# Optimization experiments

Measured on AMD Instinct MI355X. Metric: run time of the kernel, lower is better.

Reference implementation:

```python
import jax, jax.numpy as jnp
import numpy as np

D, H, FFN_D, B, LT, LS = 1024, 16, 4096, 4, 1024, 1024
EPS = 1e-5  # torch LayerNorm default
NEG = -10000000000.0


def setup_inputs() -> dict:
    key = jax.random.key(0)
    ks = iter(jax.random.split(key, 64))
    s = 0.02
    n = lambda shape: jax.random.normal(next(ks), shape, jnp.float32) * s
    inp = {
        'enc_output': n((LS, B, D)),
        'embedded': n((LT, B, D)),
        'src_mask': jnp.zeros((LS, B), jnp.bool_),
        'tgt_mask': jnp.zeros((LT, B), jnp.bool_),
    }
    for p in ('mmha', 'ed'):
        for w in ('q', 'k', 'v', 'o'):
            inp[f'{p}_w{w}'] = n((D, D))
            inp[f'{p}_b{w}'] = jnp.zeros((D,), jnp.float32)
    inp['ffn_w1'] = n((FFN_D, D)); inp['ffn_b1'] = jnp.zeros((FFN_D,), jnp.float32)
    inp['ffn_w2'] = n((D, FFN_D)); inp['ffn_b2'] = jnp.zeros((D,), jnp.float32)
    for i in range(3):
        inp[f'ln{i}_g'] = jnp.ones((D,), jnp.float32)
        inp[f'ln{i}_b'] = jnp.zeros((D,), jnp.float32)
    return inp


def _ln(x, g, b):
    m = x.mean(-1, keepdims=True)
    v = ((x - m) ** 2).mean(-1, keepdims=True)
    return (x - m) / jnp.sqrt(v + EPS) * g + b


def _mha(qx, kx, vx, wq, bq, wk, bk, wv, bv, wo, bo, mask):
    # qx: (Lq,B,D); kx,vx: (Lk,B,D); mask broadcastable to (B,H,Lq,Lk), True=masked
    Lq, Bn, Dm = qx.shape
    dk = Dm // H
    proj = lambda x, w, bb: (x @ w.T + bb).reshape(x.shape[0], Bn, H, dk).transpose(1, 2, 0, 3)
    q, k, v = proj(qx, wq, bq), proj(kx, wk, bk), proj(vx, wv, bv)  # (B,H,L,dk)
    scores = jnp.einsum('bhqd,bhkd->bhqk', q, k) / np.float32(np.sqrt(dk))
    scores = jnp.where(mask, NEG, scores)  # masked_fill semantics
    w = jax.nn.softmax(scores, axis=-1)  # dropout is identity in eval
    attn = jnp.einsum('bhqk,bhkd->bhqd', w, v).transpose(2, 0, 1, 3).reshape(Lq, Bn, Dm)
    return attn @ wo.T + bo


def reference(enc_output, embedded, src_mask, tgt_mask,
              mmha_wq, mmha_bq, mmha_wk, mmha_bk, mmha_wv, mmha_bv, mmha_wo, mmha_bo,
              ed_wq, ed_bq, ed_wk, ed_bk, ed_wv, ed_bv, ed_wo, ed_bo,
              ffn_w1, ffn_b1, ffn_w2, ffn_b2,
              ln0_g, ln0_b, ln1_g, ln1_b, ln2_g, ln2_b):
    Lt = embedded.shape[0]
    causal = jnp.triu(jnp.ones((Lt, Lt), jnp.bool_), 1)[None, None]      # (1,1,Lt,Lt)
    tmask = tgt_mask.T[:, None, None, :]                                  # (B,1,1,Lt)
    # Sublayer 0: masked self-attention (computed but UNUSED downstream,
    # faithfully mirroring the original forward which discards self_attn).
    self_attn = embedded + _mha(_ln(embedded, ln0_g, ln0_b), _ln(embedded, ln0_g, ln0_b), _ln(embedded, ln0_g, ln0_b),
                                mmha_wq, mmha_bq, mmha_wk, mmha_bk, mmha_wv, mmha_bv, mmha_wo, mmha_bo,
                                causal | tmask)
    del self_attn
    # Sublayer 1: enc-dec attention; residual input is `embedded` (as in source).
    smask = src_mask.T[:, None, None, :]                                  # (B,1,1,Ls)
    q_in = _ln(embedded, ln1_g, ln1_b)
    enc_dec = embedded + _mha(q_in, enc_output, enc_output,
                              ed_wq, ed_bq, ed_wk, ed_bk, ed_wv, ed_bv, ed_wo, ed_bo,
                              smask)
    # Sublayer 2: FFN
    z = _ln(enc_dec, ln2_g, ln2_b)
    ffn = jnp.maximum(z @ ffn_w1.T + ffn_b1, 0.0) @ ffn_w2.T + ffn_b2
    return enc_dec + ffn
```

## Files before the change

### kernel.cpp

```cpp
#include <hip/hip_runtime.h>
#include <cstdint>
#include <math.h>

constexpr int NH  = 16;
constexpr int DKH = 64;
constexpr int SEQ = 1024;
constexpr int NB  = 4;
constexpr int DM  = 1024;
constexpr int DF  = 4096;

typedef __bf16 bf16;
typedef __bf16 bf16x4 __attribute__((ext_vector_type(4)));
typedef __bf16 bf16x8 __attribute__((ext_vector_type(8)));
typedef float  f32x4  __attribute__((ext_vector_type(4)));

#define MFMA16(a, b, c) __builtin_amdgcn_mfma_f32_16x16x32_bf16((a), (b), (c), 0, 0, 0)

__device__ __forceinline__ void gload_lds16(const void* g, void* l) {
  __builtin_amdgcn_global_load_lds(
      (const __attribute__((address_space(1))) unsigned int*)(uintptr_t)g,
      (__attribute__((address_space(3))) unsigned int*)(uintptr_t)l,
      16, 0, 0);
}

template <int BK>
__device__ __forceinline__ int swz(int row) {
  return (BK == 32) ? ((row >> 1) & 3) : (row & 7);
}

template <int ROWS, int BK>
__device__ __forceinline__ void stage_tile(const bf16* __restrict__ g, int ldg,
                                           bf16* __restrict__ l, int t) {
  constexpr int ITER = ROWS * BK / 2048;
#pragma unroll
  for (int i = 0; i < ITER; ++i) {
    const int off = (i * 256 + t) * 8;
    const int row = off / BK;
    const int cc = (off & (BK - 1)) >> 3;
    const int sc = cc ^ swz<BK>(row);
    gload_lds16(&g[(size_t)row * ldg + (sc << 3)], &l[off]);
  }
}

__global__ __launch_bounds__(256) void cast4_kernel(const float* __restrict__ i0, const float* __restrict__ i1,
                                                    const float* __restrict__ i2, const float* __restrict__ i3,
                                                    bf16* __restrict__ o0, bf16* __restrict__ o1,
                                                    bf16* __restrict__ o2, bf16* __restrict__ o3) {
  const int sel = blockIdx.x >> 10;
  const int idx = (blockIdx.x & 1023) * 256 + threadIdx.x;
  const float* in = sel == 0 ? i0 : sel == 1 ? i1 : sel == 2 ? i2 : i3;
  bf16* out = sel == 0 ? o0 : sel == 1 ? o1 : sel == 2 ? o2 : o3;
  const float4 v = ((const float4*)in)[idx];
  bf16x4 ov;
  ov[0] = (bf16)v.x; ov[1] = (bf16)v.y; ov[2] = (bf16)v.z; ov[3] = (bf16)v.w;
  ((bf16x4*)out)[idx] = ov;
}

__global__ __launch_bounds__(256) void cast3_kernel(const float* __restrict__ i0, const float* __restrict__ i1,
                                                    const float* __restrict__ i2,
                                                    bf16* __restrict__ o0, bf16* __restrict__ o1,
                                                    bf16* __restrict__ o2) {
  const int sel = blockIdx.x >> 12;
  const int idx = (blockIdx.x & 4095) * 256 + threadIdx.x;
  const float* in = sel == 0 ? i0 : sel == 1 ? i1 : i2;
  bf16* out = sel == 0 ? o0 : sel == 1 ? o1 : o2;
  const float4 v = ((const float4*)in)[idx];
  bf16x4 ov;
  ov[0] = (bf16)v.x; ov[1] = (bf16)v.y; ov[2] = (bf16)v.z; ov[3] = (bf16)v.w;
  ((bf16x4*)out)[idx] = ov;
}

__global__ __launch_bounds__(256) void ln_kernel(const float* __restrict__ x,
                                                 const float* __restrict__ gam,
                                                 const float* __restrict__ bet,
                                                 bf16* __restrict__ out) {
  const int row = blockIdx.x, t = threadIdx.x;
  const float4 v = ((const float4*)(x + (size_t)row * DM))[t];
  float s  = v.x + v.y + v.z + v.w;
  float s2 = v.x * v.x + v.y * v.y + v.z * v.z + v.w * v.w;
#pragma unroll
  for (int m = 1; m < 64; m <<= 1) { s += __shfl_xor(s, m); s2 += __shfl_xor(s2, m); }
  __shared__ float red[8];
  const int w = t >> 6;
  if ((t & 63) == 0) { red[w] = s; red[4 + w] = s2; }
  __syncthreads();
  s  = red[0] + red[1] + red[2] + red[3];
  s2 = red[4] + red[5] + red[6] + red[7];
  const float mean = s * (1.f / DM);
  const float var  = s2 * (1.f / DM) - mean * mean;
  const float rstd = rsqrtf(var + 1e-5f);
  const float4 g4 = ((const float4*)gam)[t];
  const float4 b4 = ((const float4*)bet)[t];
  bf16x4 ov;
  ov[0] = (bf16)((v.x - mean) * rstd * g4.x + b4.x);
  ov[1] = (bf16)((v.y - mean) * rstd * g4.y + b4.y);
  ov[2] = (bf16)((v.z - mean) * rstd * g4.z + b4.z);
  ov[3] = (bf16)((v.w - mean) * rstd * g4.w + b4.w);
  ((bf16x4*)(out + (size_t)row * DM))[t] = ov;
}

enum { EPI_QKV = 0, EPI_O = 3, EPI_F1 = 4, EPI_F2 = 5 };

struct GParams {
  const bf16* A;
  const bf16* A2;
  const bf16* W;
  const float* b0;
  const float* b1;
  const float* b2;
  const float* resid;
  void* out;
  void* out1;
  void* out2;
  int N;
  int K;
};

template <int MODE, int BN, int BK>
__global__ __launch_bounds__(256, 3) void gemm2(GParams p) {
  constexpr int BM = 128;
  constexpr int WTM = (BN == 128) ? 64 : 32;
  constexpr int MI = WTM / 16;
  __shared__ __align__(16) bf16 As[2][BM * BK];
  __shared__ __align__(16) bf16 Bs[2][BN * BK];
  const int t = threadIdx.x, lane = t & 63, w = t >> 6;
  const int lr = lane & 15, lg = lane >> 4;
  const int wr = (BN == 128) ? (w >> 1) : w;
  const int wc = (BN == 128) ? (w & 1) : 0;
  const int m0 = blockIdx.x * BM, n0 = blockIdx.y * BN;
  const bf16* Ap = (MODE == EPI_QKV && n0 >= 1024) ? p.A2 : p.A;
  const f32x4 FZ = {0.f, 0.f, 0.f, 0.f};
  f32x4 acc[MI][4];
#pragma unroll
  for (int i = 0; i < MI; ++i)
#pragma unroll
    for (int j = 0; j < 4; ++j) acc[i][j] = FZ;

  const int nk = p.K / BK;
  stage_tile<BM, BK>(&Ap[(size_t)m0 * p.K], p.K, As[0], t);
  stage_tile<BN, BK>(&p.W[(size_t)n0 * p.K], p.K, Bs[0], t);
  asm volatile("s_waitcnt vmcnt(0)" ::: "memory");
  __syncthreads();

  int cur = 0;
  for (int kt = 0; kt < nk; ++kt) {
    if (kt + 1 < nk) {
      stage_tile<BM, BK>(&Ap[(size_t)m0 * p.K + (size_t)(kt + 1) * BK], p.K, As[cur ^ 1], t);
      stage_tile<BN, BK>(&p.W[(size_t)n0 * p.K + (size_t)(kt + 1) * BK], p.K, Bs[cur ^ 1], t);
    }
    const bf16* Asl = As[cur];
    const bf16* Bsl = Bs[cur];
#pragma unroll
    for (int kh = 0; kh < BK / 32; ++kh) {
      bf16x8 af[MI], bfr[4];
#pragma unroll
      for (int i = 0; i < MI; ++i) {
        const int row = wr * WTM + i * 16 + lr;
        const int c = (kh * 4 + lg) ^ swz<BK>(row);
        af[i] = *(const bf16x8*)&Asl[row * BK + c * 8];
      }
#pragma unroll
      for (int j = 0; j < 4; ++j) {
        const int row = wc * 64 + j * 16 + lr;
        const int c = (kh * 4 + lg) ^ swz<BK>(row);
        bfr[j] = *(const bf16x8*)&Bsl[row * BK + c * 8];
      }
#pragma unroll
      for (int i = 0; i < MI; ++i)
#pragma unroll
        for (int j = 0; j < 4; ++j) acc[i][j] = MFMA16(af[i], bfr[j], acc[i][j]);
    }
    asm volatile("s_waitcnt vmcnt(0)" ::: "memory");
    __syncthreads();
    cur ^= 1;
  }

#pragma unroll
  for (int i = 0; i < MI; ++i) {
#pragma unroll
    for (int j = 0; j < 4; ++j) {
      const int c = n0 + wc * 64 + j * 16 + lr;
      float bj;
      if constexpr (MODE == EPI_QKV)
        bj = (c < 1024 ? p.b0 : c < 2048 ? p.b1 : p.b2)[c & 1023];
      else
        bj = p.b0[c];
#pragma unroll
      for (int g = 0; g < 4; ++g) {
        const int r = m0 + wr * WTM + i * 16 + 4 * lg + g;
        float v = acc[i][j][g] + bj;
        if constexpr (MODE == EPI_QKV) {
          const int cl = c & 1023;
          const size_t sidx = (((size_t)((r & 3) * NH + (cl >> 6)) << 10) + (r >> 2)) * DKH + (cl & 63);
          if (c < 1024)
            ((bf16*)p.out)[sidx] = (bf16)(v * 0.125f);
          else if (c < 2048)
            ((bf16*)p.out1)[sidx] = (bf16)v;
          else
            ((bf16*)p.out2)[(((size_t)((r & 3) * NH + (cl >> 6)) * DKH + (cl & 63)) << 10) + (r >> 2)] = (bf16)v;
        } else if constexpr (MODE == EPI_O) {
          const size_t idx = (size_t)r * p.N + c;
          ((float*)p.out)[idx] = v + p.resid[idx];
        } else if constexpr (MODE == EPI_F1) {
          ((bf16*)p.out)[(size_t)r * p.N + c] = (bf16)fmaxf(v, 0.f);
        } else {
          const size_t idx = (size_t)r * p.N + c;
          ((float*)p.out)[idx] = v + p.resid[idx];
        }
      }
    }
  }
}

__global__ __launch_bounds__(256) void attn_kernel(const bf16* __restrict__ Qg,
                                                   const bf16* __restrict__ Kg,
                                                   const bf16* __restrict__ Vtg,
                                                   const unsigned char* __restrict__ smask,
                                                   bf16* __restrict__ Og) {
  __shared__ __align__(16) bf16 Ks[4096];
  __shared__ __align__(16) bf16 Vs[4096];
  __shared__ __align__(16) bf16 Ps[4][2304];
  const int t = threadIdx.x, lane = t & 63, w = t >> 6;
  const int lr = lane & 15, lg = lane >> 4;
  const int bh = blockIdx.y, b = bh >> 4, h = bh & 15;
  const int q0 = blockIdx.x * 128 + w * 32;
  const size_t base = (size_t)bh << 16;

  bf16x8 qa[2][2];
#pragma unroll
  for (int m = 0; m < 2; ++m)
#pragma unroll
    for (int c = 0; c < 2; ++c)
      qa[m][c] = *(const bf16x8*)&Qg[base + (size_t)(q0 + m * 16 + lr) * DKH + c * 32 + lg * 8];

  const f32x4 FZ = {0.f, 0.f, 0.f, 0.f};
  f32x4 o[2][4];
  float mrun[2][4], lrun[2][4];
#pragma unroll
  for (int m = 0; m < 2; ++m)
#pragma unroll
    for (int g = 0; g < 4; ++g) { mrun[m][g] = -INFINITY; lrun[m][g] = 0.f; }
#pragma unroll
  for (int m = 0; m < 2; ++m)
#pragma unroll
    for (int n = 0; n < 4; ++n) o[m][n] = FZ;

  for (int kt = 0; kt < SEQ / 64; ++kt) {
    const int kv0 = kt * 64;
#pragma unroll
    for (int i = 0; i < 2; ++i) {
      const int off = (i * 256 + t) * 8;
      const int hi = off >> 11, mid = (off >> 5) & 63, lo = off & 31;
      gload_lds16(&Kg[base + (size_t)(kv0 + mid) * DKH + hi * 32 + lo], &Ks[off]);
      gload_lds16(&Vtg[base + (size_t)mid * SEQ + kv0 + hi * 32 + lo], &Vs[off]);
    }
    asm volatile("s_waitcnt vmcnt(0)" ::: "memory");
    __syncthreads();

    bf16x8 kb[4][2], vb[4][2];
#pragma unroll
    for (int n = 0; n < 4; ++n)
#pragma unroll
      for (int c = 0; c < 2; ++c) {
        kb[n][c] = *(const bf16x8*)&Ks[c * 2048 + (n * 16 + lr) * 32 + lg * 8];
        vb[n][c] = *(const bf16x8*)&Vs[c * 2048 + (n * 16 + lr) * 32 + lg * 8];
      }

    f32x4 s[2][4];
#pragma unroll
    for (int m = 0; m < 2; ++m)
#pragma unroll
      for (int n = 0; n < 4; ++n) s[m][n] = FZ;
#pragma unroll
    for (int c = 0; c < 2; ++c)
#pragma unroll
      for (int m = 0; m < 2; ++m)
#pragma unroll
        for (int n = 0; n < 4; ++n) s[m][n] = MFMA16(qa[m][c], kb[n][c], s[m][n]);

    float madd[4];
#pragma unroll
    for (int n = 0; n < 4; ++n)
      madd[n] = smask[(size_t)(kv0 + n * 16 + lr) * NB + b] ? -1e10f : 0.f;
#pragma unroll
    for (int m = 0; m < 2; ++m)
#pragma unroll
      for (int n = 0; n < 4; ++n)
#pragma unroll
        for (int g = 0; g < 4; ++g) s[m][n][g] += madd[n];

#pragma unroll
    for (int m = 0; m < 2; ++m) {
#pragma unroll
      for (int g = 0; g < 4; ++g) {
        float tm = fmaxf(fmaxf(s[m][0][g], s[m][1][g]), fmaxf(s[m][2][g], s[m][3][g]));
        tm = fmaxf(tm, __shfl_xor(tm, 1));
        tm = fmaxf(tm, __shfl_xor(tm, 2));
        tm = fmaxf(tm, __shfl_xor(tm, 4));
        tm = fmaxf(tm, __shfl_xor(tm, 8));
        const float mnew = fmaxf(mrun[m][g], tm);
        float ts = 0.f;
#pragma unroll
        for (int n = 0; n < 4; ++n) {
          const float p = __expf(s[m][n][g] - mnew);
          s[m][n][g] = p;
          ts += p;
        }
        ts += __shfl_xor(ts, 1);
        ts += __shfl_xor(ts, 2);
        ts += __shfl_xor(ts, 4);
        ts += __shfl_xor(ts, 8);
        const float sc = __expf(mrun[m][g] - mnew);
        lrun[m][g] = lrun[m][g] * sc + ts;
        mrun[m][g] = mnew;
#pragma unroll
        for (int n = 0; n < 4; ++n) o[m][n][g] *= sc;
      }
    }

    bf16* Pw = &Ps[w][0];
#pragma unroll
    for (int m = 0; m < 2; ++m)
#pragma unroll
      for (int n = 0; n < 4; ++n)
#pragma unroll
        for (int g = 0; g < 4; ++g)
          Pw[(m * 16 + 4 * lg + g) * 72 + n * 16 + lr] = (bf16)s[m][n][g];
    __builtin_amdgcn_sched_barrier(0);

#pragma unroll
    for (int c = 0; c < 2; ++c) {
      bf16x8 pa[2];
#pragma unroll
      for (int m = 0; m < 2; ++m)
        pa[m] = *(const bf16x8*)&Pw[(m * 16 + lr) * 72 + c * 32 + lg * 8];
#pragma unroll
      for (int m = 0; m < 2; ++m)
#pragma unroll
        for (int n = 0; n < 4; ++n) o[m][n] = MFMA16(pa[m], vb[n][c], o[m][n]);
    }
    __syncthreads();
  }

#pragma unroll
  for (int m = 0; m < 2; ++m)
#pragma unroll
    for (int g = 0; g < 4; ++g) {
      const int l = q0 + m * 16 + 4 * lg + g;
      const float inv = 1.0f / lrun[m][g];
#pragma unroll
      for (int n = 0; n < 4; ++n)
        Og[(size_t)(l * NB + b) * DM + h * 64 + n * 16 + lr] = (bf16)(o[m][n][g] * inv);
    }
}

extern "C" void kernel_launch(void* const* d_in, const int* in_sizes, int n_in,
                              void* d_out, int out_size, void* d_ws, size_t ws_size,
                              hipStream_t stream) {
  const float* enc = (const float*)d_in[0];
  const float* emb = (const float*)d_in[1];
  const unsigned char* smask = (const unsigned char*)d_in[2];
  const float* wq = (const float*)d_in[12]; const float* bq = (const float*)d_in[13];
  const float* wk = (const float*)d_in[14]; const float* bk = (const float*)d_in[15];
  const float* wv = (const float*)d_in[16]; const float* bv = (const float*)d_in[17];
  const float* wo = (const float*)d_in[18]; const float* bo = (const float*)d_in[19];
  const float* w1 = (const float*)d_in[20]; const float* b1 = (const float*)d_in[21];
  const float* w2 = (const float*)d_in[22]; const float* b2 = (const float*)d_in[23];
  const float* g1 = (const float*)d_in[26]; const float* be1 = (const float*)d_in[27];
  const float* g2 = (const float*)d_in[28]; const float* be2 = (const float*)d_in[29];

  char* ws = (char*)d_ws;
  const size_t MB = (size_t)1 << 20;
  bf16* wqkv_bf = (bf16*)(ws + 0 * MB);
  bf16* wo_bf   = (bf16*)(ws + 6 * MB);
  bf16* w1_bf   = (bf16*)(ws + 8 * MB);
  bf16* w2_bf   = (bf16*)(ws + 16 * MB);
  bf16* enc_bf  = (bf16*)(ws + 24 * MB);
  bf16* z_bf    = enc_bf;
  bf16* qin_bf  = (bf16*)(ws + 32 * MB);
  bf16* attn_bf = qin_bf;
  bf16* Q_bf    = (bf16*)(ws + 40 * MB);
  bf16* K_bf    = (bf16*)(ws + 48 * MB);
  bf16* Vt_bf   = (bf16*)(ws + 56 * MB);
  float* encdec = (float*)(ws + 64 * MB);
  bf16* h_bf    = (bf16*)(ws + 80 * MB);

  cast4_kernel<<<4096, 256, 0, stream>>>(wq, wk, wv, wo,
                                         wqkv_bf, wqkv_bf + (1 << 20), wqkv_bf + (2 << 20), wo_bf);
  cast3_kernel<<<12288, 256, 0, stream>>>(w1, w2, enc, w1_bf, w2_bf, enc_bf);

  ln_kernel<<<4096, 256, 0, stream>>>(emb, g1, be1, qin_bf);

  {
    GParams p{qin_bf, enc_bf, wqkv_bf, bq, bk, bv, nullptr, Q_bf, K_bf, Vt_bf, 3072, DM};
    gemm2<EPI_QKV, 128, 32><<<dim3(32, 24), 256, 0, stream>>>(p);
  }

  attn_kernel<<<dim3(8, 64), 256, 0, stream>>>(Q_bf, K_bf, Vt_bf, smask, attn_bf);

  {
    GParams p{attn_bf, nullptr, wo_bf, bo, nullptr, nullptr, emb, encdec, nullptr, nullptr, DM, DM};
    gemm2<EPI_O, 64, 64><<<dim3(32, 16), 256, 0, stream>>>(p);
  }

  ln_kernel<<<4096, 256, 0, stream>>>(encdec, g2, be2, z_bf);

  {
    GParams p{z_bf, nullptr, w1_bf, b1, nullptr, nullptr, nullptr, h_bf, nullptr, nullptr, DF, DM};
    gemm2<EPI_F1, 128, 32><<<dim3(32, 32), 256, 0, stream>>>(p);
  }
  {
    GParams p{h_bf, nullptr, w2_bf, b2, nullptr, nullptr, encdec, d_out, nullptr, nullptr, DM, DF};
    gemm2<EPI_F2, 64, 64><<<dim3(32, 16), 256, 0, stream>>>(p);
  }
}
```

Before: 398.7 us.

## Double-buffer K/V in attention, use 8 waves with 16 rows each

Restructures the attention kernel to 512 threads per block, with each wave owning 16 query rows instead of 32. K/V tiles are double-buffered in LDS and the next tile is prefetched while the current one is computed. The grid is flattened and remapped so that neighbouring blocks share a head group, which may help L2 reuse. MFMA sections are wrapped in setprio. The intent is to hide global-to-LDS load latency behind compute and raise occupancy. In exchange, the K/V LDS traffic per query row doubles, because each wave now reads the full tile for only 16 rows.

```diff
diff --git a/kernel.cpp b/kernel.cpp
--- a/kernel.cpp
+++ b/kernel.cpp
@@ -212,146 +212,137 @@
   }
 }
 
-__global__ __launch_bounds__(256) void attn_kernel(const bf16* __restrict__ Qg,
-                                                   const bf16* __restrict__ Kg,
-                                                   const bf16* __restrict__ Vtg,
-                                                   const unsigned char* __restrict__ smask,
-                                                   bf16* __restrict__ Og) {
-  __shared__ __align__(16) bf16 Ks[4096];
-  __shared__ __align__(16) bf16 Vs[4096];
-  __shared__ __align__(16) bf16 Ps[4][2304];
+__global__ __launch_bounds__(512, 4) void attn_kernel(const bf16* __restrict__ Qg,
+                                                      const bf16* __restrict__ Kg,
+                                                      const bf16* __restrict__ Vtg,
+                                                      const unsigned char* __restrict__ smask,
+                                                      bf16* __restrict__ Og) {
+  __shared__ __align__(16) bf16 Ks[2][4096];
+  __shared__ __align__(16) bf16 Vs[2][4096];
+  __shared__ __align__(16) bf16 Ps[8][1152];
   const int t = threadIdx.x, lane = t & 63, w = t >> 6;
   const int lr = lane & 15, lg = lane >> 4;
-  const int bh = blockIdx.y, b = bh >> 4, h = bh & 15;
-  const int q0 = blockIdx.x * 128 + w * 32;
+  const int id = blockIdx.x;
+  const int bh = ((id >> 6) << 3) | (id & 7);
+  const int qt = (id >> 3) & 7;
+  const int b = bh >> 4, h = bh & 15;
+  const int q0 = qt * 128 + w * 16;
   const size_t base = (size_t)bh << 16;
 
-  bf16x8 qa[2][2];
-#pragma unroll
-  for (int m = 0; m < 2; ++m)
-#pragma unroll
-    for (int c = 0; c < 2; ++c)
-      qa[m][c] = *(const bf16x8*)&Qg[base + (size_t)(q0 + m * 16 + lr) * DKH + c * 32 + lg * 8];
+  bf16x8 qa[2];
+#pragma unroll
+  for (int c = 0; c < 2; ++c)
+    qa[c] = *(const bf16x8*)&Qg[base + (size_t)(q0 + lr) * DKH + c * 32 + lg * 8];
 
   const f32x4 FZ = {0.f, 0.f, 0.f, 0.f};
-  f32x4 o[2][4];
-  float mrun[2][4], lrun[2][4];
-#pragma unroll
-  for (int m = 0; m < 2; ++m)
-#pragma unroll
-    for (int g = 0; g < 4; ++g) { mrun[m][g] = -INFINITY; lrun[m][g] = 0.f; }
-#pragma unroll
-  for (int m = 0; m < 2; ++m)
-#pragma unroll
-    for (int n = 0; n < 4; ++n) o[m][n] = FZ;
-
+  f32x4 o[4];
+  float mrun[4], lrun[4];
+#pragma unroll
+  for (int g = 0; g < 4; ++g) { mrun[g] = -INFINITY; lrun[g] = 0.f; o[g] = FZ; }
+
+  {
+    const int off = t * 8;
+    const int hi = off >> 11, mid = (off >> 5) & 63, lo = off & 31;
+    gload_lds16(&Kg[base + (size_t)mid * DKH + hi * 32 + lo], &Ks[0][off]);
+    gload_lds16(&Vtg[base + (size_t)mid * SEQ + hi * 32 + lo], &Vs[0][off]);
+  }
+  asm volatile("s_waitcnt vmcnt(0)" ::: "memory");
+  __syncthreads();
+
+  int cur = 0;
   for (int kt = 0; kt < SEQ / 64; ++kt) {
     const int kv0 = kt * 64;
-#pragma unroll
-    for (int i = 0; i < 2; ++i) {
-      const int off = (i * 256 + t) * 8;
+    if (kt + 1 < SEQ / 64) {
+      const int off = t * 8;
       const int hi = off >> 11, mid = (off >> 5) & 63, lo = off & 31;
-      gload_lds16(&Kg[base + (size_t)(kv0 + mid) * DKH + hi * 32 + lo], &Ks[off]);
-      gload_lds16(&Vtg[base + (size_t)mid * SEQ + kv0 + hi * 32 + lo], &Vs[off]);
-    }
+      gload_lds16(&Kg[base + (size_t)(kv0 + 64 + mid) * DKH + hi * 32 + lo], &Ks[cur ^ 1][off]);
+      gload_lds16(&Vtg[base + (size_t)mid * SEQ + kv0 + 64 + hi * 32 + lo], &Vs[cur ^ 1][off]);
+    }
+
+    f32x4 s[4];
+#pragma unroll
+    for (int n = 0; n < 4; ++n) s[n] = FZ;
+#pragma unroll
+    for (int c = 0; c < 2; ++c) {
+      bf16x8 kb[4];
+#pragma unroll
+      for (int n = 0; n < 4; ++n)
+        kb[n] = *(const bf16x8*)&Ks[cur][c * 2048 + (n * 16 + lr) * 32 + lg * 8];
+      __builtin_amdgcn_s_setprio(1);
+#pragma unroll
+      for (int n = 0; n < 4; ++n) s[n] = MFMA16(qa[c], kb[n], s[n]);
+      __builtin_amdgcn_s_setprio(0);
+    }
+
+    float madd[4];
+#pragma unroll
+    for (int n = 0; n < 4; ++n)
+      madd[n] = smask[(size_t)(kv0 + n * 16 + lr) * NB + b] ? -1e10f : 0.f;
+#pragma unroll
+    for (int n = 0; n < 4; ++n)
+#pragma unroll
+      for (int g = 0; g < 4; ++g) s[n][g] += madd[n];
+
+#pragma unroll
+    for (int g = 0; g < 4; ++g) {
+      float tm = fmaxf(fmaxf(s[0][g], s[1][g]), fmaxf(s[2][g], s[3][g]));
+      tm = fmaxf(tm, __shfl_xor(tm, 1));
+      tm = fmaxf(tm, __shfl_xor(tm, 2));
+      tm = fmaxf(tm, __shfl_xor(tm, 4));
+      tm = fmaxf(tm, __shfl_xor(tm, 8));
+      const float mnew = fmaxf(mrun[g], tm);
+      float ts = 0.f;
+#pragma unroll
+      for (int n = 0; n < 4; ++n) {
+        const float p = __expf(s[n][g] - mnew);
+        s[n][g] = p;
+        ts += p;
+      }
+      ts += __shfl_xor(ts, 1);
+      ts += __shfl_xor(ts, 2);
+      ts += __shfl_xor(ts, 4);
+      ts += __shfl_xor(ts, 8);
+      const float sc = __expf(mrun[g] - mnew);
+      lrun[g] = lrun[g] * sc + ts;
+      mrun[g] = mnew;
+#pragma unroll
+      for (int n = 0; n < 4; ++n) o[n][g] *= sc;
+    }
+
+    bf16* Pw = &Ps[w][0];
+#pragma unroll
+    for (int n = 0; n < 4; ++n)
+#pragma unroll
+      for (int g = 0; g < 4; ++g)
+        Pw[(4 * lg + g) * 72 + n * 16 + lr] = (bf16)s[n][g];
+    __builtin_amdgcn_sched_barrier(0);
+
+#pragma unroll
+    for (int c = 0; c < 2; ++c) {
+      const bf16x8 pa = *(const bf16x8*)&Pw[lr * 72 + c * 32 + lg * 8];
+      bf16x8 vb[4];
+#pragma unroll
+      for (int n = 0; n < 4; ++n)
+        vb[n] = *(const bf16x8*)&Vs[cur][c * 2048 + (n * 16 + lr) * 32 + lg * 8];
+      __builtin_amdgcn_s_setprio(1);
+#pragma unroll
+      for (int n = 0; n < 4; ++n) o[n] = MFMA16(pa, vb[n], o[n]);
+      __builtin_amdgcn_s_setprio(0);
+    }
+
     asm volatile("s_waitcnt vmcnt(0)" ::: "memory");
     __syncthreads();
-
-    bf16x8 kb[4][2], vb[4][2];
+    cur ^= 1;
+  }
+
+#pragma unroll
+  for (int g = 0; g < 4; ++g) {
+    const int l = q0 + 4 * lg + g;
+    const float inv = 1.0f / lrun[g];
 #pragma unroll
     for (int n = 0; n < 4; ++n)
-#pragma unroll
-      for (int c = 0; c < 2; ++c) {
-        kb[n][c] = *(const bf16x8*)&Ks[c * 2048 + (n * 16 + lr) * 32 + lg * 8];
-        vb[n][c] = *(const bf16x8*)&Vs[c * 2048 + (n * 16 + lr) * 32 + lg * 8];
-      }
-
-    f32x4 s[2][4];
-#pragma unroll
-    for (int m = 0; m < 2; ++m)
-#pragma unroll
-      for (int n = 0; n < 4; ++n) s[m][n] = FZ;
-#pragma unroll
-    for (int c = 0; c < 2; ++c)
-#pragma unroll
-      for (int m = 0; m < 2; ++m)
-#pragma unroll
-        for (int n = 0; n < 4; ++n) s[m][n] = MFMA16(qa[m][c], kb[n][c], s[m][n]);
-
-    float madd[4];
-#pragma unroll
-    for (int n = 0; n < 4; ++n)
-      madd[n] = smask[(size_t)(kv0 + n * 16 + lr) * NB + b] ? -1e10f : 0.f;
-#pragma unroll
-    for (int m = 0; m < 2; ++m)
-#pragma unroll
-      for (int n = 0; n < 4; ++n)
-#pragma unroll
-        for (int g = 0; g < 4; ++g) s[m][n][g] += madd[n];
-
-#pragma unroll
-    for (int m = 0; m < 2; ++m) {
-#pragma unroll
-      for (int g = 0; g < 4; ++g) {
-        float tm = fmaxf(fmaxf(s[m][0][g], s[m][1][g]), fmaxf(s[m][2][g], s[m][3][g]));
-        tm = fmaxf(tm, __shfl_xor(tm, 1));
-        tm = fmaxf(tm, __shfl_xor(tm, 2));
-        tm = fmaxf(tm, __shfl_xor(tm, 4));
-        tm = fmaxf(tm, __shfl_xor(tm, 8));
-        const float mnew = fmaxf(mrun[m][g], tm);
-        float ts = 0.f;
-#pragma unroll
-        for (int n = 0; n < 4; ++n) {
-          const float p = __expf(s[m][n][g] - mnew);
-          s[m][n][g] = p;
-          ts += p;
-        }
-        ts += __shfl_xor(ts, 1);
-        ts += __shfl_xor(ts, 2);
-        ts += __shfl_xor(ts, 4);
-        ts += __shfl_xor(ts, 8);
-        const float sc = __expf(mrun[m][g] - mnew);
-        lrun[m][g] = lrun[m][g] * sc + ts;
-        mrun[m][g] = mnew;
-#pragma unroll
-        for (int n = 0; n < 4; ++n) o[m][n][g] *= sc;
-      }
-    }
-
-    bf16* Pw = &Ps[w][0];
-#pragma unroll
-    for (int m = 0; m < 2; ++m)
-#pragma unroll
-      for (int n = 0; n < 4; ++n)
-#pragma unroll
-        for (int g = 0; g < 4; ++g)
-          Pw[(m * 16 + 4 * lg + g) * 72 + n * 16 + lr] = (bf16)s[m][n][g];
-    __builtin_amdgcn_sched_barrier(0);
-
-#pragma unroll
-    for (int c = 0; c < 2; ++c) {
-      bf16x8 pa[2];
-#pragma unroll
-      for (int m = 0; m < 2; ++m)
-        pa[m] = *(const bf16x8*)&Pw[(m * 16 + lr) * 72 + c * 32 + lg * 8];
-#pragma unroll
-      for (int m = 0; m < 2; ++m)
-#pragma unroll
-        for (int n = 0; n < 4; ++n) o[m][n] = MFMA16(pa[m], vb[n][c], o[m][n]);
-    }
-    __syncthreads();
-  }
-
-#pragma unroll
-  for (int m = 0; m < 2; ++m)
-#pragma unroll
-    for (int g = 0; g < 4; ++g) {
-      const int l = q0 + m * 16 + 4 * lg + g;
-      const float inv = 1.0f / lrun[m][g];
-#pragma unroll
-      for (int n = 0; n < 4; ++n)
-        Og[(size_t)(l * NB + b) * DM + h * 64 + n * 16 + lr] = (bf16)(o[m][n][g] * inv);
-    }
+      Og[(size_t)(l * NB + b) * DM + h * 64 + n * 16 + lr] = (bf16)(o[n][g] * inv);
+  }
 }
 
 extern "C" void kernel_launch(void* const* d_in, const int* in_sizes, int n_in,
@@ -396,7 +387,7 @@
     gemm2<EPI_QKV, 128, 32><<<dim3(32, 24), 256, 0, stream>>>(p);
   }
 
-  attn_kernel<<<dim3(8, 64), 256, 0, stream>>>(Q_bf, K_bf, Vt_bf, smask, attn_bf);
+  attn_kernel<<<512, 512, 0, stream>>>(Q_bf, K_bf, Vt_bf, smask, attn_bf);
 
   {
     GParams p{attn_bf, nullptr, wo_bf, bo, nullptr, nullptr, emb, encdec, nullptr, nullptr, DM, DM};
```

Measured after the change: 388.3 us. 2.6% less time.
